# Kernel tuning notes

Measured on AMD Instinct MI355X. Metric: run time of the kernel, lower is better.

## Reference

```python
import jax, jax.numpy as jnp
import numpy as np

N_NODES = 50000
N_EDGES = 800000
NEG_SLOPE = 0.2


def _edge_softmax(scores, dst, n):
    # scores: [E, H]; softmax over edges grouped by destination node
    m = jax.ops.segment_max(scores, dst, num_segments=n)          # [N, H]
    ex = jnp.exp(scores - m[dst])                                 # [E, H]
    s = jax.ops.segment_sum(ex, dst, num_segments=n)              # [N, H]
    return ex / s[dst]


def _gat_layer(h, W, attn_l, attn_r, bias, src, dst, n, heads, out_d):
    feat = (h @ W).reshape(n, heads, out_d)                       # [N, H, D]
    el = jnp.sum(feat * attn_l, axis=-1)                          # [N, H]
    er = jnp.sum(feat * attn_r, axis=-1)                          # [N, H]
    e = jax.nn.leaky_relu(el[src] + er[dst], NEG_SLOPE)           # [E, H]
    alpha = _edge_softmax(e, dst, n)                              # [E, H]
    msg = feat[src] * alpha[:, :, None]                           # [E, H, D]
    rst = jax.ops.segment_sum(msg, dst, num_segments=n)           # [N, H, D]
    return rst + bias.reshape(1, heads, out_d)


def setup_inputs() -> dict:
    key = jax.random.key(0)
    ks = jax.random.split(key, 12)
    in_dim, hid, heads, out_dim = 128, 64, 4, 64
    sc = 0.1
    return {
        "emb": jax.random.normal(ks[0], (N_NODES, in_dim), jnp.float32),
        "src": jax.random.randint(ks[1], (N_EDGES,), 0, N_NODES, jnp.int32),
        "dst": jax.random.randint(ks[2], (N_EDGES,), 0, N_NODES, jnp.int32),
        "W1": jax.random.normal(ks[3], (in_dim, heads * hid), jnp.float32) * sc,
        "attn_l1": jax.random.normal(ks[4], (1, heads, hid), jnp.float32) * sc,
        "attn_r1": jax.random.normal(ks[5], (1, heads, hid), jnp.float32) * sc,
        "b1": jax.random.normal(ks[6], (heads * hid,), jnp.float32) * sc,
        "W2": jax.random.normal(ks[7], (heads * hid, out_dim), jnp.float32) * sc,
        "attn_l2": jax.random.normal(ks[8], (1, 1, out_dim), jnp.float32) * sc,
        "attn_r2": jax.random.normal(ks[9], (1, 1, out_dim), jnp.float32) * sc,
        "b2": jax.random.normal(ks[10], (out_dim,), jnp.float32) * sc,
    }


def reference(emb, src, dst, W1, attn_l1, attn_r1, b1, W2, attn_l2, attn_r2, b2):
    n = emb.shape[0]
    h = _gat_layer(emb, W1, attn_l1, attn_r1, b1, src, dst, n, 4, 64)   # [N,4,64]
    h = jax.nn.relu(h).reshape(n, 4 * 64)                                # [N,256]
    h = _gat_layer(h, W2, attn_l2, attn_r2, b2, src, dst, n, 1, 64)      # [N,1,64]
    return h.reshape(n, 64)
```

## Files before the change

kernel.cpp:

```cpp
#include <hip/hip_runtime.h>
#include <hip/hip_bf16.h>
#include <math.h>

#define DIV_UP(a,b) (((a)+(b)-1)/(b))

typedef __attribute__((ext_vector_type(8))) short short8v;
typedef __attribute__((ext_vector_type(4))) float f32x4;

__device__ __forceinline__ float bf_lo(unsigned u){ union{unsigned x; float f;} v; v.x = u << 16; return v.f; }
__device__ __forceinline__ float bf_hi(unsigned u){ union{unsigned x; float f;} v; v.x = u & 0xffff0000u; return v.f; }
__device__ __forceinline__ unsigned short f2bf(float f){
  union{float f; unsigned u;} v; v.f = f;
  unsigned r = v.u + 0x7fff + ((v.u >> 16) & 1);
  return (unsigned short)(r >> 16);
}
__device__ __forceinline__ unsigned packbf(float a, float b){
  return (unsigned)f2bf(a) | ((unsigned)f2bf(b) << 16);
}
__device__ __forceinline__ float lrelu(float x){ return x > 0.f ? x : 0.2f*x; }

__global__ __launch_bounds__(256) void k_scan1(const int* __restrict__ deg,
                                               int* __restrict__ blocksum, int N){
  int b = blockIdx.x;
  int base = b*1024 + threadIdx.x*4;
  int s = 0;
  if (base + 3 < N){
    int4 v = *(const int4*)&deg[base];
    s = v.x + v.y + v.z + v.w;
  } else {
    for (int i = 0; i < 4; i++){ int idx = base + i; if (idx < N) s += deg[idx]; }
  }
  #pragma unroll
  for (int o = 32; o; o >>= 1) s += __shfl_down(s, o);
  __shared__ int ws[4];
  int wid = threadIdx.x >> 6, lane = threadIdx.x & 63;
  if (lane == 0) ws[wid] = s;
  __syncthreads();
  if (threadIdx.x == 0) blocksum[b] = ws[0] + ws[1] + ws[2] + ws[3];
}

__global__ __launch_bounds__(256) void k_scan3(const int* __restrict__ deg,
                                               const int* __restrict__ blocksum, int nb,
                                               int* __restrict__ row_start,
                                               int* __restrict__ cursor, int N){
  int b = blockIdx.x;
  __shared__ int s_boff;
  if (threadIdx.x < 64){
    int acc = 0;
    for (int base = 0; base < nb; base += 64){
      int idx = base + threadIdx.x;
      if (idx < nb && idx < b) acc += blocksum[idx];
    }
    #pragma unroll
    for (int o = 32; o; o >>= 1) acc += __shfl_down(acc, o);
    if (threadIdx.x == 0) s_boff = acc;
  }
  int base = b*1024 + threadIdx.x*4;
  int v[4];
  #pragma unroll
  for (int i = 0; i < 4; i++){ int idx = base + i; v[i] = (idx < N) ? deg[idx] : 0; }
  int s = v[0] + v[1] + v[2] + v[3];
  int lane = threadIdx.x & 63, wid = threadIdx.x >> 6;
  int inc = s;
  #pragma unroll
  for (int o = 1; o < 64; o <<= 1){ int t = __shfl_up(inc, o); if (lane >= o) inc += t; }
  __shared__ int wsum[4];
  if (lane == 63) wsum[wid] = inc;
  __syncthreads();
  int woff = 0;
  #pragma unroll
  for (int i = 0; i < 4; i++) if (i < wid) woff += wsum[i];
  int run = s_boff + woff + inc - s;
  #pragma unroll
  for (int i = 0; i < 4; i++){
    int idx = base + i;
    if (idx < N){ row_start[idx] = run; cursor[idx] = run; run += v[i]; }
  }
  if (base < N && base + 4 >= N) row_start[N] = run;
}

__global__ void k_fillw4(const int* __restrict__ dst, const int* __restrict__ src,
                         int* __restrict__ cursor, int* __restrict__ srcp,
                         const float4* __restrict__ el4, const float4* __restrict__ er4,
                         float4* __restrict__ w4, int E){
  int i = blockIdx.x*blockDim.x + threadIdx.x;
  if (i < E){
    int d = dst[i], s = src[i];
    int p = atomicAdd(&cursor[d], 1);
    srcp[p] = s;
    float4 l = el4[s], r = er4[d];
    float4 w;
    w.x = __expf(lrelu(l.x + r.x));
    w.y = __expf(lrelu(l.y + r.y));
    w.z = __expf(lrelu(l.z + r.z));
    w.w = __expf(lrelu(l.w + r.w));
    w4[p] = w;
  }
}

__global__ __launch_bounds__(256) void k_gemm1_count(const float* __restrict__ A,
      const float* __restrict__ B,
      unsigned short* __restrict__ Cbf,
      const float* __restrict__ al, const float* __restrict__ ar,
      float* __restrict__ el, float* __restrict__ er, int M,
      const int* __restrict__ dst, int* __restrict__ deg, int E, int gemmBlocks){
  __shared__ alignas(16) __hip_bfloat16 At[64][136];
  __shared__ alignas(16) __hip_bfloat16 Bt[64][136];
  __shared__ float elp[2][64], erp[2][64];

  if (blockIdx.x >= gemmBlocks){
    int i = (blockIdx.x - gemmBlocks)*256 + threadIdx.x;
    if (i < E) atomicAdd(&deg[dst[i]], 1);
    return;
  }

  const int tid = threadIdx.x;
  const int lane = tid & 63, w = tid >> 6;
  const int mw = w >> 1, nw = w & 1;
  const int m0 = blockIdx.x * 64;
  const int rbase = mw*32, cbase = nw*32;
  const int fr = lane & 15, fg = lane >> 4;

  #pragma unroll
  for (int i = 0; i < 8; i++){
    int q = tid + i*256;
    int row = q >> 5, c4 = q & 31;
    float4 a = make_float4(0.f,0.f,0.f,0.f);
    if (m0 + row < M) a = *(const float4*)&A[(size_t)(m0+row)*128 + c4*4];
    *(uint2*)&At[row][c4*4] = make_uint2(packbf(a.x,a.y), packbf(a.z,a.w));
  }

  for (int by = 0; by < 4; by++){
    int n0 = by * 64;
    __syncthreads();
    #pragma unroll
    for (int i = 0; i < 8; i++){
      int q = tid + i*256;
      int c = q & 63, k4 = q >> 6;
      float b0 = B[(size_t)(k4*4+0)*256 + n0 + c];
      float b1 = B[(size_t)(k4*4+1)*256 + n0 + c];
      float b2 = B[(size_t)(k4*4+2)*256 + n0 + c];
      float b3 = B[(size_t)(k4*4+3)*256 + n0 + c];
      *(uint2*)&Bt[c][k4*4] = make_uint2(packbf(b0,b1), packbf(b2,b3));
    }
    __syncthreads();

    f32x4 acc[2][2];
    #pragma unroll
    for (int i = 0; i < 2; i++)
      #pragma unroll
      for (int jj = 0; jj < 2; jj++)
        #pragma unroll
        for (int r = 0; r < 4; r++) acc[i][jj][r] = 0.f;

    #pragma unroll
    for (int ks = 0; ks < 4; ks++){
      short8v a0 = *(const short8v*)&At[rbase + fr     ][ks*32 + fg*8];
      short8v a1 = *(const short8v*)&At[rbase + 16 + fr][ks*32 + fg*8];
      short8v b0 = *(const short8v*)&Bt[cbase + fr     ][ks*32 + fg*8];
      short8v b1 = *(const short8v*)&Bt[cbase + 16 + fr][ks*32 + fg*8];
      acc[0][0] = __builtin_amdgcn_mfma_f32_16x16x32_bf16(a0, b0, acc[0][0], 0,0,0);
      acc[0][1] = __builtin_amdgcn_mfma_f32_16x16x32_bf16(a0, b1, acc[0][1], 0,0,0);
      acc[1][0] = __builtin_amdgcn_mfma_f32_16x16x32_bf16(a1, b0, acc[1][0], 0,0,0);
      acc[1][1] = __builtin_amdgcn_mfma_f32_16x16x32_bf16(a1, b1, acc[1][1], 0,0,0);
    }

    float alv[2], arv[2];
    #pragma unroll
    for (int nt = 0; nt < 2; nt++){
      int col = cbase + nt*16 + fr;
      alv[nt] = al[n0 + col];
      arv[nt] = ar[n0 + col];
    }
    #pragma unroll
    for (int mt = 0; mt < 2; mt++){
      #pragma unroll
      for (int r = 0; r < 4; r++){
        float pl = acc[mt][0][r]*alv[0] + acc[mt][1][r]*alv[1];
        float pr = acc[mt][0][r]*arv[0] + acc[mt][1][r]*arv[1];
        #pragma unroll
        for (int o = 1; o < 16; o <<= 1){ pl += __shfl_xor(pl, o); pr += __shfl_xor(pr, o); }
        if (fr == 0){
          int rl = rbase + mt*16 + fg*4 + r;
          elp[nw][rl] = pl; erp[nw][rl] = pr;
        }
      }
    }
    #pragma unroll
    for (int mt = 0; mt < 2; mt++){
      #pragma unroll
      for (int r = 0; r < 4; r++){
        int row = m0 + rbase + mt*16 + fg*4 + r;
        if (row < M){
          #pragma unroll
          for (int nt = 0; nt < 2; nt++)
            Cbf[(size_t)row*256 + n0 + cbase + nt*16 + fr] = f2bf(acc[mt][nt][r]);
        }
      }
    }
    __syncthreads();
    if (tid < 64){
      int row = m0 + tid;
      if (row < M){
        el[(size_t)row*4 + by] = elp[0][tid] + elp[1][tid];
        er[(size_t)row*4 + by] = erp[0][tid] + erp[1][tid];
      }
    }
  }
}

template<int K, int H, bool ABF>
__global__ __launch_bounds__(256) void k_gemm_mfma(const void* __restrict__ Av,
      const float* __restrict__ B, int ldb,
      unsigned short* __restrict__ Cbf,
      const float* __restrict__ al, const float* __restrict__ ar,
      float* __restrict__ el, float* __restrict__ er, int M){
  constexpr int KP = K + 8;
  __shared__ alignas(16) __hip_bfloat16 At[64][KP];
  __shared__ alignas(16) __hip_bfloat16 Bt[64][KP];
  __shared__ float elp[2][64], erp[2][64];
  const int tid = threadIdx.x;
  const int lane = tid & 63, w = tid >> 6;
  const int mw = w >> 1, nw = w & 1;
  const int m0 = blockIdx.x * 64, by = blockIdx.y, n0 = by * 64;

  if constexpr (!ABF){
    const float* A = (const float*)Av;
    #pragma unroll
    for (int i = 0; i < K/16; i++){
      int q = tid + i*256;
      int row = q / (K/4), c4 = q % (K/4);
      float4 a = make_float4(0.f,0.f,0.f,0.f);
      if (m0 + row < M) a = *(const float4*)&A[(size_t)(m0+row)*K + c4*4];
      *(uint2*)&At[row][c4*4] = make_uint2(packbf(a.x,a.y), packbf(a.z,a.w));
    }
  } else {
    const __hip_bfloat16* A = (const __hip_bfloat16*)Av;
    #pragma unroll
    for (int i = 0; i < K/32; i++){
      int q = tid + i*256;
      int row = q / (K/8), c8 = q % (K/8);
      uint4 u = make_uint4(0,0,0,0);
      if (m0 + row < M) u = *(const uint4*)&A[(size_t)(m0+row)*K + c8*8];
      *(uint4*)&At[row][c8*8] = u;
    }
  }
  #pragma unroll
  for (int i = 0; i < K/16; i++){
    int q = tid + i*256;
    int c = q & 63, k4 = q >> 6;
    float b0 = B[(size_t)(k4*4+0)*ldb + n0 + c];
    float b1 = B[(size_t)(k4*4+1)*ldb + n0 + c];
    float b2 = B[(size_t)(k4*4+2)*ldb + n0 + c];
    float b3 = B[(size_t)(k4*4+3)*ldb + n0 + c];
    *(uint2*)&Bt[c][k4*4] = make_uint2(packbf(b0,b1), packbf(b2,b3));
  }
  __syncthreads();

  f32x4 acc[2][2];
  #pragma unroll
  for (int i = 0; i < 2; i++)
    #pragma unroll
    for (int j = 0; j < 2; j++)
      #pragma unroll
      for (int r = 0; r < 4; r++) acc[i][j][r] = 0.f;

  const int rbase = mw*32, cbase = nw*32;
  const int fr = lane & 15, fg = lane >> 4;
  #pragma unroll
  for (int ks = 0; ks < K/32; ks++){
    short8v a0 = *(const short8v*)&At[rbase + fr     ][ks*32 + fg*8];
    short8v a1 = *(const short8v*)&At[rbase + 16 + fr][ks*32 + fg*8];
    short8v b0 = *(const short8v*)&Bt[cbase + fr     ][ks*32 + fg*8];
    short8v b1 = *(const short8v*)&Bt[cbase + 16 + fr][ks*32 + fg*8];
    acc[0][0] = __builtin_amdgcn_mfma_f32_16x16x32_bf16(a0, b0, acc[0][0], 0,0,0);
    acc[0][1] = __builtin_amdgcn_mfma_f32_16x16x32_bf16(a0, b1, acc[0][1], 0,0,0);
    acc[1][0] = __builtin_amdgcn_mfma_f32_16x16x32_bf16(a1, b0, acc[1][0], 0,0,0);
    acc[1][1] = __builtin_amdgcn_mfma_f32_16x16x32_bf16(a1, b1, acc[1][1], 0,0,0);
  }

  float alv[2], arv[2];
  #pragma unroll
  for (int nt = 0; nt < 2; nt++){
    int col = cbase + nt*16 + fr;
    alv[nt] = al[by*64 + col];
    arv[nt] = ar[by*64 + col];
  }
  #pragma unroll
  for (int mt = 0; mt < 2; mt++){
    #pragma unroll
    for (int r = 0; r < 4; r++){
      float pl = acc[mt][0][r]*alv[0] + acc[mt][1][r]*alv[1];
      float pr = acc[mt][0][r]*arv[0] + acc[mt][1][r]*arv[1];
      #pragma unroll
      for (int o = 1; o < 16; o <<= 1){ pl += __shfl_xor(pl, o); pr += __shfl_xor(pr, o); }
      if (fr == 0){
        int rl = rbase + mt*16 + fg*4 + r;
        elp[nw][rl] = pl; erp[nw][rl] = pr;
      }
    }
  }
  const int NN = H*64;
  #pragma unroll
  for (int mt = 0; mt < 2; mt++){
    #pragma unroll
    for (int r = 0; r < 4; r++){
      int row = m0 + rbase + mt*16 + fg*4 + r;
      if (row < M){
        #pragma unroll
        for (int nt = 0; nt < 2; nt++)
          Cbf[(size_t)row*NN + n0 + cbase + nt*16 + fr] = f2bf(acc[mt][nt][r]);
      }
    }
  }
  __syncthreads();
  if (tid < 64){
    int row = m0 + tid;
    if (row < M){
      el[(size_t)row*H + by] = elp[0][tid] + elp[1][tid];
      er[(size_t)row*H + by] = erp[0][tid] + erp[1][tid];
    }
  }
}

__global__ __launch_bounds__(256) void k_gath4(const uint4* __restrict__ fbase,
      const float* __restrict__ w4, const int* __restrict__ row_start,
      const int* __restrict__ srcp, const float* __restrict__ bias,
      __hip_bfloat16* __restrict__ outb, int N, int nwaves){
  int wv = threadIdx.x >> 6, lane = threadIdx.x & 63;
  int g = lane >> 4, j = lane & 15, h = j >> 2;
  const unsigned jo2 = (unsigned)(j << 1);

  int n = blockIdx.x*4 + wv;
  if (n >= N) return;
  int rs = row_start[n], re = row_start[n+1];

  while (true){
    int deg = re - rs;
    int nn = n + nwaves;
    int rs_n = 0, re_n = 0;
    if (nn < N){ rs_n = row_start[nn]; re_n = row_start[nn+1]; }

    float acc[16];
    #pragma unroll
    for (int k = 0; k < 16; k++) acc[k] = 0.f;
    float Sacc = 0.f;

    int i = 0;
    int full = deg & ~15;
    for (; i < full; i += 16){
      float wb[4]; uint4 u0[4], u1[4];
      #pragma unroll
      for (int k = 0; k < 4; k++){
        unsigned e = (unsigned)(rs + i + k*4 + g);
        int sb = srcp[e];
        wb[k] = w4[(e << 2) + h];
        unsigned fi = ((unsigned)sb << 5) + jo2;
        u0[k] = fbase[fi];
        u1[k] = fbase[fi + 1];
      }
      #pragma unroll
      for (int k = 0; k < 4; k++){
        float wk = wb[k];
        Sacc += wk;
        acc[0]  += bf_lo(u0[k].x)*wk; acc[1]  += bf_hi(u0[k].x)*wk;
        acc[2]  += bf_lo(u0[k].y)*wk; acc[3]  += bf_hi(u0[k].y)*wk;
        acc[4]  += bf_lo(u0[k].z)*wk; acc[5]  += bf_hi(u0[k].z)*wk;
        acc[6]  += bf_lo(u0[k].w)*wk; acc[7]  += bf_hi(u0[k].w)*wk;
        acc[8]  += bf_lo(u1[k].x)*wk; acc[9]  += bf_hi(u1[k].x)*wk;
        acc[10] += bf_lo(u1[k].y)*wk; acc[11] += bf_hi(u1[k].y)*wk;
        acc[12] += bf_lo(u1[k].z)*wk; acc[13] += bf_hi(u1[k].z)*wk;
        acc[14] += bf_lo(u1[k].w)*wk; acc[15] += bf_hi(u1[k].w)*wk;
      }
    }
    if (i < deg){
      float wb[4]; uint4 u0[4], u1[4];
      #pragma unroll
      for (int k = 0; k < 4; k++){
        int e = i + k*4 + g;
        wb[k] = 0.f;
        u0[k] = make_uint4(0,0,0,0); u1[k] = make_uint4(0,0,0,0);
        if (e < deg){
          unsigned ee = (unsigned)(rs + e);
          int sb = srcp[ee];
          wb[k] = w4[(ee << 2) + h];
          unsigned fi = ((unsigned)sb << 5) + jo2;
          u0[k] = fbase[fi];
          u1[k] = fbase[fi + 1];
        }
      }
      #pragma unroll
      for (int k = 0; k < 4; k++){
        float wk = wb[k];
        Sacc += wk;
        acc[0]  += bf_lo(u0[k].x)*wk; acc[1]  += bf_hi(u0[k].x)*wk;
        acc[2]  += bf_lo(u0[k].y)*wk; acc[3]  += bf_hi(u0[k].y)*wk;
        acc[4]  += bf_lo(u0[k].z)*wk; acc[5]  += bf_hi(u0[k].z)*wk;
        acc[6]  += bf_lo(u0[k].w)*wk; acc[7]  += bf_hi(u0[k].w)*wk;
        acc[8]  += bf_lo(u1[k].x)*wk; acc[9]  += bf_hi(u1[k].x)*wk;
        acc[10] += bf_lo(u1[k].y)*wk; acc[11] += bf_hi(u1[k].y)*wk;
        acc[12] += bf_lo(u1[k].z)*wk; acc[13] += bf_hi(u1[k].z)*wk;
        acc[14] += bf_lo(u1[k].w)*wk; acc[15] += bf_hi(u1[k].w)*wk;
      }
    }

    #pragma unroll
    for (int k = 0; k < 16; k++){
      acc[k] += __shfl_xor(acc[k], 16);
      acc[k] += __shfl_xor(acc[k], 32);
    }
    Sacc += __shfl_xor(Sacc, 16);
    Sacc += __shfl_xor(Sacc, 32);
    if (g == 0){
      float inv = (deg > 0 && Sacc > 0.f) ? 1.f / Sacc : 0.f;
      float4 b0 = *(const float4*)&bias[j*16 + 0];
      float4 b1 = *(const float4*)&bias[j*16 + 4];
      float4 b2 = *(const float4*)&bias[j*16 + 8];
      float4 b3 = *(const float4*)&bias[j*16 + 12];
      float v[16];
      v[0]=acc[0]*inv+b0.x;  v[1]=acc[1]*inv+b0.y;  v[2]=acc[2]*inv+b0.z;  v[3]=acc[3]*inv+b0.w;
      v[4]=acc[4]*inv+b1.x;  v[5]=acc[5]*inv+b1.y;  v[6]=acc[6]*inv+b1.z;  v[7]=acc[7]*inv+b1.w;
      v[8]=acc[8]*inv+b2.x;  v[9]=acc[9]*inv+b2.y;  v[10]=acc[10]*inv+b2.z; v[11]=acc[11]*inv+b2.w;
      v[12]=acc[12]*inv+b3.x; v[13]=acc[13]*inv+b3.y; v[14]=acc[14]*inv+b3.z; v[15]=acc[15]*inv+b3.w;
      #pragma unroll
      for (int k = 0; k < 16; k++) v[k] = fmaxf(v[k], 0.f);
      uint4 o0, o1;
      o0.x = packbf(v[0], v[1]);   o0.y = packbf(v[2], v[3]);
      o0.z = packbf(v[4], v[5]);   o0.w = packbf(v[6], v[7]);
      o1.x = packbf(v[8], v[9]);   o1.y = packbf(v[10], v[11]);
      o1.z = packbf(v[12], v[13]); o1.w = packbf(v[14], v[15]);
      uint4* op = (uint4*)outb + (size_t)n*32 + (j << 1);
      op[0] = o0; op[1] = o1;
    }

    if (nn >= N) break;
    n = nn; rs = rs_n; re = re_n;
  }
}

__global__ __launch_bounds__(256) void k_gath1(const uint2* __restrict__ fbase,
      const float* __restrict__ el2, const float* __restrict__ er2,
      const int* __restrict__ row_start, const int* __restrict__ srcp,
      const float* __restrict__ bias, float* __restrict__ out, int N, int nwaves){
  int wv = threadIdx.x >> 6, lane = threadIdx.x & 63;
  int g = lane >> 4, j = lane & 15;
  const unsigned jo = (unsigned)j;

  int n = blockIdx.x*4 + wv;
  if (n >= N) return;
  int rs = row_start[n], re = row_start[n+1];

  while (true){
    int deg = re - rs;
    int nn = n + nwaves;
    int rs_n = 0, re_n = 0;
    if (nn < N){ rs_n = row_start[nn]; re_n = row_start[nn+1]; }

    float ern = er2[n];
    float acc[4] = {0.f, 0.f, 0.f, 0.f};
    float Sacc = 0.f;

    int i = 0;
    int full = deg & ~15;
    for (; i < full; i += 16){
      float wb[4]; uint2 u[4];
      #pragma unroll
      for (int k = 0; k < 4; k++){
        unsigned e = (unsigned)(rs + i + k*4 + g);
        int sb = srcp[e];
        float x = el2[sb] + ern;
        x = x > 0.f ? x : 0.2f*x;
        wb[k] = __expf(x);
        u[k] = fbase[((unsigned)sb << 4) + jo];
      }
      #pragma unroll
      for (int k = 0; k < 4; k++){
        float wk = wb[k];
        Sacc += wk;
        acc[0] += bf_lo(u[k].x)*wk; acc[1] += bf_hi(u[k].x)*wk;
        acc[2] += bf_lo(u[k].y)*wk; acc[3] += bf_hi(u[k].y)*wk;
      }
    }
    if (i < deg){
      float wb[4]; uint2 u[4];
      #pragma unroll
      for (int k = 0; k < 4; k++){
        int e = i + k*4 + g;
        wb[k] = 0.f;
        u[k] = make_uint2(0,0);
        if (e < deg){
          unsigned ee = (unsigned)(rs + e);
          int sb = srcp[ee];
          float x = el2[sb] + ern;
          x = x > 0.f ? x : 0.2f*x;
          wb[k] = __expf(x);
          u[k] = fbase[((unsigned)sb << 4) + jo];
        }
      }
      #pragma unroll
      for (int k = 0; k < 4; k++){
        float wk = wb[k];
        Sacc += wk;
        acc[0] += bf_lo(u[k].x)*wk; acc[1] += bf_hi(u[k].x)*wk;
        acc[2] += bf_lo(u[k].y)*wk; acc[3] += bf_hi(u[k].y)*wk;
      }
    }

    #pragma unroll
    for (int k = 0; k < 4; k++){
      acc[k] += __shfl_xor(acc[k], 16);
      acc[k] += __shfl_xor(acc[k], 32);
    }
    Sacc += __shfl_xor(Sacc, 16);
    Sacc += __shfl_xor(Sacc, 32);
    if (g == 0){
      float inv = (deg > 0 && Sacc > 0.f) ? 1.f / Sacc : 0.f;
      float4 b = *(const float4*)&bias[j*4];
      float4 o;
      o.x = acc[0]*inv + b.x; o.y = acc[1]*inv + b.y;
      o.z = acc[2]*inv + b.z; o.w = acc[3]*inv + b.w;
      *(float4*)&out[(size_t)n*64 + j*4] = o;
    }

    if (nn >= N) break;
    n = nn; rs = rs_n; re = re_n;
  }
}

extern "C" void kernel_launch(void* const* d_in, const int* in_sizes, int n_in,
                              void* d_out, int out_size, void* d_ws, size_t ws_size,
                              hipStream_t stream) {
  const float* emb = (const float*)d_in[0];
  const int*   src = (const int*)d_in[1];
  const int*   dst = (const int*)d_in[2];
  const float* W1  = (const float*)d_in[3];
  const float* al1 = (const float*)d_in[4];
  const float* ar1 = (const float*)d_in[5];
  const float* b1  = (const float*)d_in[6];
  const float* W2  = (const float*)d_in[7];
  const float* al2 = (const float*)d_in[8];
  const float* ar2 = (const float*)d_in[9];
  const float* b2  = (const float*)d_in[10];
  float* out = (float*)d_out;

  const int N = in_sizes[0] / 128;
  const int E = in_sizes[1];

  char* p = (char*)d_ws;
  auto alloc = [&](size_t bytes) -> void* {
    void* r = (void*)p; p += (bytes + 255) & ~(size_t)255; return r;
  };
  __hip_bfloat16* feat1b = (__hip_bfloat16*)alloc((size_t)N*256*2);
  __hip_bfloat16* h1b    = (__hip_bfloat16*)alloc((size_t)N*256*2);
  __hip_bfloat16* feat2b = (__hip_bfloat16*)alloc((size_t)N*64*2);
  float* el1             = (float*)alloc((size_t)N*4*4);
  float* er1             = (float*)alloc((size_t)N*4*4);
  float* el2             = (float*)alloc((size_t)N*4);
  float* er2             = (float*)alloc((size_t)N*4);
  int*   deg             = (int*)alloc((size_t)N*4);
  int*   row_start       = (int*)alloc((size_t)(N+1)*4);
  int*   cursor          = (int*)alloc((size_t)N*4);
  int*   blocksum        = (int*)alloc((size_t)DIV_UP(N,1024)*4);
  int*   srcp            = (int*)alloc((size_t)E*4);
  float* w4              = (float*)alloc((size_t)E*16);

  const int nb = DIV_UP(N, 1024);
  const int gblocks = min(DIV_UP(N, 4), 2048);
  const int nwaves  = gblocks * 4;
  const int gemmBlocks = DIV_UP(N, 64);
  const int cntBlocks  = DIV_UP(E, 256);

  hipMemsetAsync(deg, 0, (size_t)N*4, stream);

  k_gemm1_count<<<gemmBlocks + cntBlocks, 256, 0, stream>>>(
      emb, W1, (unsigned short*)feat1b, al1, ar1, el1, er1, N,
      dst, deg, E, gemmBlocks);

  k_scan1<<<nb, 256, 0, stream>>>(deg, blocksum, N);
  k_scan3<<<nb, 256, 0, stream>>>(deg, blocksum, nb, row_start, cursor, N);
  k_fillw4<<<DIV_UP(E,256), 256, 0, stream>>>(dst, src, cursor, srcp,
      (const float4*)el1, (const float4*)er1, (float4*)w4, E);

  k_gath4<<<gblocks, 256, 0, stream>>>((const uint4*)feat1b, w4, row_start,
                                       srcp, b1, h1b, N, nwaves);
  k_gemm_mfma<256,1,true><<<dim3(DIV_UP(N,64), 1), 256, 0, stream>>>(
      h1b, W2, 64, (unsigned short*)feat2b, al2, ar2, el2, er2, N);
  k_gath1<<<gblocks, 256, 0, stream>>>((const uint2*)feat2b, el2, er2,
                                       row_start, srcp, b2, out, N, nwaves);
}
```

Baseline: 200.0 us.

## Split gather kernels by feature column chunks and store edge weights per head

Edge attention weights are now stored head-major (one plane per head) instead of interleaved float4. Both aggregation kernels split the feature dimension into column chunks handled by separate blocks, so each wave covers 16 or 32 edges per iteration with a single 16-byte load per lane rather than several loads per lane. The aim is to cut register pressure and improve load coalescing. In exchange, srcp and the edge indices are re-read once per chunk, there are more shuffle reduction steps, and the grid sizes change.

```diff
diff --git a/kernel.cpp b/kernel.cpp
--- a/kernel.cpp
+++ b/kernel.cpp
@@ -82,19 +82,17 @@
 __global__ void k_fillw4(const int* __restrict__ dst, const int* __restrict__ src,
                          int* __restrict__ cursor, int* __restrict__ srcp,
                          const float4* __restrict__ el4, const float4* __restrict__ er4,
-                         float4* __restrict__ w4, int E){
+                         float* __restrict__ w4T, int E){
   int i = blockIdx.x*blockDim.x + threadIdx.x;
   if (i < E){
     int d = dst[i], s = src[i];
     int p = atomicAdd(&cursor[d], 1);
     srcp[p] = s;
     float4 l = el4[s], r = er4[d];
-    float4 w;
-    w.x = __expf(lrelu(l.x + r.x));
-    w.y = __expf(lrelu(l.y + r.y));
-    w.z = __expf(lrelu(l.z + r.z));
-    w.w = __expf(lrelu(l.w + r.w));
-    w4[p] = w;
+    w4T[0*E + p] = __expf(lrelu(l.x + r.x));
+    w4T[1*E + p] = __expf(lrelu(l.y + r.y));
+    w4T[2*E + p] = __expf(lrelu(l.z + r.z));
+    w4T[3*E + p] = __expf(lrelu(l.w + r.w));
   }
 }
 
@@ -323,15 +321,18 @@
   }
 }
 
-__global__ __launch_bounds__(256) void k_gath4(const uint4* __restrict__ fbase,
-      const float* __restrict__ w4, const int* __restrict__ row_start,
+__global__ __launch_bounds__(256) void k_gath4s(const uint4* __restrict__ fbase,
+      const float* __restrict__ w4T, const int* __restrict__ row_start,
       const int* __restrict__ srcp, const float* __restrict__ bias,
-      __hip_bfloat16* __restrict__ outb, int N, int nwaves){
+      __hip_bfloat16* __restrict__ outb, int N, int E, int nwaves){
   int wv = threadIdx.x >> 6, lane = threadIdx.x & 63;
-  int g = lane >> 4, j = lane & 15, h = j >> 2;
-  const unsigned jo2 = (unsigned)(j << 1);
-
-  int n = blockIdx.x*4 + wv;
+  int c = blockIdx.x & 7;
+  int h = c >> 1;
+  int el_ = lane >> 2, s = lane & 3;
+  const float* wplane = w4T + (size_t)h*E;
+  const unsigned cbase = (unsigned)(c << 2);
+
+  int n = (blockIdx.x >> 3)*4 + wv;
   if (n >= N) return;
   int rs = row_start[n], re = row_start[n+1];
 
@@ -341,96 +342,64 @@
     int rs_n = 0, re_n = 0;
     if (nn < N){ rs_n = row_start[nn]; re_n = row_start[nn+1]; }
 
-    float acc[16];
-    #pragma unroll
-    for (int k = 0; k < 16; k++) acc[k] = 0.f;
+    float acc[8];
+    #pragma unroll
+    for (int k = 0; k < 8; k++) acc[k] = 0.f;
     float Sacc = 0.f;
 
     int i = 0;
     int full = deg & ~15;
     for (; i < full; i += 16){
-      float wb[4]; uint4 u0[4], u1[4];
-      #pragma unroll
-      for (int k = 0; k < 4; k++){
-        unsigned e = (unsigned)(rs + i + k*4 + g);
-        int sb = srcp[e];
-        wb[k] = w4[(e << 2) + h];
-        unsigned fi = ((unsigned)sb << 5) + jo2;
-        u0[k] = fbase[fi];
-        u1[k] = fbase[fi + 1];
-      }
-      #pragma unroll
-      for (int k = 0; k < 4; k++){
-        float wk = wb[k];
-        Sacc += wk;
-        acc[0]  += bf_lo(u0[k].x)*wk; acc[1]  += bf_hi(u0[k].x)*wk;
-        acc[2]  += bf_lo(u0[k].y)*wk; acc[3]  += bf_hi(u0[k].y)*wk;
-        acc[4]  += bf_lo(u0[k].z)*wk; acc[5]  += bf_hi(u0[k].z)*wk;
-        acc[6]  += bf_lo(u0[k].w)*wk; acc[7]  += bf_hi(u0[k].w)*wk;
-        acc[8]  += bf_lo(u1[k].x)*wk; acc[9]  += bf_hi(u1[k].x)*wk;
-        acc[10] += bf_lo(u1[k].y)*wk; acc[11] += bf_hi(u1[k].y)*wk;
-        acc[12] += bf_lo(u1[k].z)*wk; acc[13] += bf_hi(u1[k].z)*wk;
-        acc[14] += bf_lo(u1[k].w)*wk; acc[15] += bf_hi(u1[k].w)*wk;
-      }
+      unsigned ee = (unsigned)(rs + i + el_);
+      int sb = srcp[ee];
+      float w = wplane[ee];
+      uint4 u = fbase[((unsigned)sb << 5) + cbase + s];
+      Sacc += w;
+      acc[0] += bf_lo(u.x)*w; acc[1] += bf_hi(u.x)*w;
+      acc[2] += bf_lo(u.y)*w; acc[3] += bf_hi(u.y)*w;
+      acc[4] += bf_lo(u.z)*w; acc[5] += bf_hi(u.z)*w;
+      acc[6] += bf_lo(u.w)*w; acc[7] += bf_hi(u.w)*w;
     }
     if (i < deg){
-      float wb[4]; uint4 u0[4], u1[4];
-      #pragma unroll
-      for (int k = 0; k < 4; k++){
-        int e = i + k*4 + g;
-        wb[k] = 0.f;
-        u0[k] = make_uint4(0,0,0,0); u1[k] = make_uint4(0,0,0,0);
-        if (e < deg){
-          unsigned ee = (unsigned)(rs + e);
-          int sb = srcp[ee];
-          wb[k] = w4[(ee << 2) + h];
-          unsigned fi = ((unsigned)sb << 5) + jo2;
-          u0[k] = fbase[fi];
-          u1[k] = fbase[fi + 1];
-        }
-      }
-      #pragma unroll
-      for (int k = 0; k < 4; k++){
-        float wk = wb[k];
-        Sacc += wk;
-        acc[0]  += bf_lo(u0[k].x)*wk; acc[1]  += bf_hi(u0[k].x)*wk;
-        acc[2]  += bf_lo(u0[k].y)*wk; acc[3]  += bf_hi(u0[k].y)*wk;
-        acc[4]  += bf_lo(u0[k].z)*wk; acc[5]  += bf_hi(u0[k].z)*wk;
-        acc[6]  += bf_lo(u0[k].w)*wk; acc[7]  += bf_hi(u0[k].w)*wk;
-        acc[8]  += bf_lo(u1[k].x)*wk; acc[9]  += bf_hi(u1[k].x)*wk;
-        acc[10] += bf_lo(u1[k].y)*wk; acc[11] += bf_hi(u1[k].y)*wk;
-        acc[12] += bf_lo(u1[k].z)*wk; acc[13] += bf_hi(u1[k].z)*wk;
-        acc[14] += bf_lo(u1[k].w)*wk; acc[15] += bf_hi(u1[k].w)*wk;
-      }
-    }
-
-    #pragma unroll
-    for (int k = 0; k < 16; k++){
-      acc[k] += __shfl_xor(acc[k], 16);
-      acc[k] += __shfl_xor(acc[k], 32);
-    }
-    Sacc += __shfl_xor(Sacc, 16);
-    Sacc += __shfl_xor(Sacc, 32);
-    if (g == 0){
+      int e = i + el_;
+      float w = 0.f; uint4 u = make_uint4(0,0,0,0);
+      if (e < deg){
+        unsigned ee = (unsigned)(rs + e);
+        int sb = srcp[ee];
+        w = wplane[ee];
+        u = fbase[((unsigned)sb << 5) + cbase + s];
+      }
+      Sacc += w;
+      acc[0] += bf_lo(u.x)*w; acc[1] += bf_hi(u.x)*w;
+      acc[2] += bf_lo(u.y)*w; acc[3] += bf_hi(u.y)*w;
+      acc[4] += bf_lo(u.z)*w; acc[5] += bf_hi(u.z)*w;
+      acc[6] += bf_lo(u.w)*w; acc[7] += bf_hi(u.w)*w;
+    }
+
+    #pragma unroll
+    for (int o = 4; o < 64; o <<= 1){
+      #pragma unroll
+      for (int k = 0; k < 8; k++) acc[k] += __shfl_xor(acc[k], o);
+      Sacc += __shfl_xor(Sacc, o);
+    }
+
+    if (el_ == 0){
       float inv = (deg > 0 && Sacc > 0.f) ? 1.f / Sacc : 0.f;
-      float4 b0 = *(const float4*)&bias[j*16 + 0];
-      float4 b1 = *(const float4*)&bias[j*16 + 4];
-      float4 b2 = *(const float4*)&bias[j*16 + 8];
-      float4 b3 = *(const float4*)&bias[j*16 + 12];
-      float v[16];
-      v[0]=acc[0]*inv+b0.x;  v[1]=acc[1]*inv+b0.y;  v[2]=acc[2]*inv+b0.z;  v[3]=acc[3]*inv+b0.w;
-      v[4]=acc[4]*inv+b1.x;  v[5]=acc[5]*inv+b1.y;  v[6]=acc[6]*inv+b1.z;  v[7]=acc[7]*inv+b1.w;
-      v[8]=acc[8]*inv+b2.x;  v[9]=acc[9]*inv+b2.y;  v[10]=acc[10]*inv+b2.z; v[11]=acc[11]*inv+b2.w;
-      v[12]=acc[12]*inv+b3.x; v[13]=acc[13]*inv+b3.y; v[14]=acc[14]*inv+b3.z; v[15]=acc[15]*inv+b3.w;
-      #pragma unroll
-      for (int k = 0; k < 16; k++) v[k] = fmaxf(v[k], 0.f);
-      uint4 o0, o1;
-      o0.x = packbf(v[0], v[1]);   o0.y = packbf(v[2], v[3]);
-      o0.z = packbf(v[4], v[5]);   o0.w = packbf(v[6], v[7]);
-      o1.x = packbf(v[8], v[9]);   o1.y = packbf(v[10], v[11]);
-      o1.z = packbf(v[12], v[13]); o1.w = packbf(v[14], v[15]);
-      uint4* op = (uint4*)outb + (size_t)n*32 + (j << 1);
-      op[0] = o0; op[1] = o1;
+      int d0 = c*32 + s*8;
+      float4 b0 = *(const float4*)&bias[d0];
+      float4 b1 = *(const float4*)&bias[d0 + 4];
+      float v0 = fmaxf(acc[0]*inv + b0.x, 0.f);
+      float v1 = fmaxf(acc[1]*inv + b0.y, 0.f);
+      float v2 = fmaxf(acc[2]*inv + b0.z, 0.f);
+      float v3 = fmaxf(acc[3]*inv + b0.w, 0.f);
+      float v4 = fmaxf(acc[4]*inv + b1.x, 0.f);
+      float v5 = fmaxf(acc[5]*inv + b1.y, 0.f);
+      float v6 = fmaxf(acc[6]*inv + b1.z, 0.f);
+      float v7 = fmaxf(acc[7]*inv + b1.w, 0.f);
+      uint4 o;
+      o.x = packbf(v0, v1); o.y = packbf(v2, v3);
+      o.z = packbf(v4, v5); o.w = packbf(v6, v7);
+      ((uint4*)outb)[(size_t)n*32 + cbase + s] = o;
     }
 
     if (nn >= N) break;
@@ -438,15 +407,16 @@
   }
 }
 
-__global__ __launch_bounds__(256) void k_gath1(const uint2* __restrict__ fbase,
+__global__ __launch_bounds__(256) void k_gath1s(const uint4* __restrict__ fbase,
       const float* __restrict__ el2, const float* __restrict__ er2,
       const int* __restrict__ row_start, const int* __restrict__ srcp,
       const float* __restrict__ bias, float* __restrict__ out, int N, int nwaves){
   int wv = threadIdx.x >> 6, lane = threadIdx.x & 63;
-  int g = lane >> 4, j = lane & 15;
-  const unsigned jo = (unsigned)j;
-
-  int n = blockIdx.x*4 + wv;
+  int c = blockIdx.x & 3;
+  int el_ = lane >> 1, s = lane & 1;
+  const unsigned cbase = (unsigned)(c << 1);
+
+  int n = (blockIdx.x >> 2)*4 + wv;
   if (n >= N) return;
   int rs = row_start[n], re = row_start[n+1];
 
@@ -457,69 +427,63 @@
     if (nn < N){ rs_n = row_start[nn]; re_n = row_start[nn+1]; }
 
     float ern = er2[n];
-    float acc[4] = {0.f, 0.f, 0.f, 0.f};
+    float acc[8];
+    #pragma unroll
+    for (int k = 0; k < 8; k++) acc[k] = 0.f;
     float Sacc = 0.f;
 
     int i = 0;
-    int full = deg & ~15;
-    for (; i < full; i += 16){
-      float wb[4]; uint2 u[4];
-      #pragma unroll
-      for (int k = 0; k < 4; k++){
-        unsigned e = (unsigned)(rs + i + k*4 + g);
-        int sb = srcp[e];
+    int full = deg & ~31;
+    for (; i < full; i += 32){
+      unsigned ee = (unsigned)(rs + i + el_);
+      int sb = srcp[ee];
+      float x = el2[sb] + ern;
+      x = x > 0.f ? x : 0.2f*x;
+      float w = __expf(x);
+      uint4 u = fbase[((unsigned)sb << 3) + cbase + s];
+      Sacc += w;
+      acc[0] += bf_lo(u.x)*w; acc[1] += bf_hi(u.x)*w;
+      acc[2] += bf_lo(u.y)*w; acc[3] += bf_hi(u.y)*w;
+      acc[4] += bf_lo(u.z)*w; acc[5] += bf_hi(u.z)*w;
+      acc[6] += bf_lo(u.w)*w; acc[7] += bf_hi(u.w)*w;
+    }
+    if (i < deg){
+      int e = i + el_;
+      float w = 0.f; uint4 u = make_uint4(0,0,0,0);
+      if (e < deg){
+        unsigned ee = (unsigned)(rs + e);
+        int sb = srcp[ee];
         float x = el2[sb] + ern;
         x = x > 0.f ? x : 0.2f*x;
-        wb[k] = __expf(x);
-        u[k] = fbase[((unsigned)sb << 4) + jo];
-      }
-      #pragma unroll
-      for (int k = 0; k < 4; k++){
-        float wk = wb[k];
-        Sacc += wk;
-        acc[0] += bf_lo(u[k].x)*wk; acc[1] += bf_hi(u[k].x)*wk;
-        acc[2] += bf_lo(u[k].y)*wk; acc[3] += bf_hi(u[k].y)*wk;
-      }
-    }
-    if (i < deg){
-      float wb[4]; uint2 u[4];
-      #pragma unroll
-      for (int k = 0; k < 4; k++){
-        int e = i + k*4 + g;
-        wb[k] = 0.f;
-        u[k] = make_uint2(0,0);
-        if (e < deg){
-          unsigned ee = (unsigned)(rs + e);
-          int sb = srcp[ee];
-          float x = el2[sb] + ern;
-          x = x > 0.f ? x : 0.2f*x;
-          wb[k] = __expf(x);
-          u[k] = fbase[((unsigned)sb << 4) + jo];
-        }
-      }
-      #pragma unroll
-      for (int k = 0; k < 4; k++){
-        float wk = wb[k];
-        Sacc += wk;
-        acc[0] += bf_lo(u[k].x)*wk; acc[1] += bf_hi(u[k].x)*wk;
-        acc[2] += bf_lo(u[k].y)*wk; acc[3] += bf_hi(u[k].y)*wk;
-      }
-    }
-
-    #pragma unroll
-    for (int k = 0; k < 4; k++){
-      acc[k] += __shfl_xor(acc[k], 16);
-      acc[k] += __shfl_xor(acc[k], 32);
-    }
-    Sacc += __shfl_xor(Sacc, 16);
-    Sacc += __shfl_xor(Sacc, 32);
-    if (g == 0){
+        w = __expf(x);
+        u = fbase[((unsigned)sb << 3) + cbase + s];
+      }
+      Sacc += w;
+      acc[0] += bf_lo(u.x)*w; acc[1] += bf_hi(u.x)*w;
+      acc[2] += bf_lo(u.y)*w; acc[3] += bf_hi(u.y)*w;
+      acc[4] += bf_lo(u.z)*w; acc[5] += bf_hi(u.z)*w;
+      acc[6] += bf_lo(u.w)*w; acc[7] += bf_hi(u.w)*w;
+    }
+
+    #pragma unroll
+    for (int o = 2; o < 64; o <<= 1){
+      #pragma unroll
+      for (int k = 0; k < 8; k++) acc[k] += __shfl_xor(acc[k], o);
+      Sacc += __shfl_xor(Sacc, o);
+    }
+
+    if (el_ == 0){
       float inv = (deg > 0 && Sacc > 0.f) ? 1.f / Sacc : 0.f;
-      float4 b = *(const float4*)&bias[j*4];
-      float4 o;
-      o.x = acc[0]*inv + b.x; o.y = acc[1]*inv + b.y;
-      o.z = acc[2]*inv + b.z; o.w = acc[3]*inv + b.w;
-      *(float4*)&out[(size_t)n*64 + j*4] = o;
+      int d0 = c*16 + s*8;
+      float4 b0 = *(const float4*)&bias[d0];
+      float4 b1 = *(const float4*)&bias[d0 + 4];
+      float4 o0, o1;
+      o0.x = acc[0]*inv + b0.x; o0.y = acc[1]*inv + b0.y;
+      o0.z = acc[2]*inv + b0.z; o0.w = acc[3]*inv + b0.w;
+      o1.x = acc[4]*inv + b1.x; o1.y = acc[5]*inv + b1.y;
+      o1.z = acc[6]*inv + b1.z; o1.w = acc[7]*inv + b1.w;
+      *(float4*)&out[(size_t)n*64 + d0] = o0;
+      *(float4*)&out[(size_t)n*64 + d0 + 4] = o1;
     }
 
     if (nn >= N) break;
@@ -562,13 +526,16 @@
   int*   cursor          = (int*)alloc((size_t)N*4);
   int*   blocksum        = (int*)alloc((size_t)DIV_UP(N,1024)*4);
   int*   srcp            = (int*)alloc((size_t)E*4);
-  float* w4              = (float*)alloc((size_t)E*16);
+  float* w4T             = (float*)alloc((size_t)E*4*4);
 
   const int nb = DIV_UP(N, 1024);
-  const int gblocks = min(DIV_UP(N, 4), 2048);
-  const int nwaves  = gblocks * 4;
   const int gemmBlocks = DIV_UP(N, 64);
   const int cntBlocks  = DIV_UP(E, 256);
+
+  const int g4nodeblk = 256;
+  const int g4nwaves  = g4nodeblk * 4;
+  const int g1nodeblk = 512;
+  const int g1nwaves  = g1nodeblk * 4;
 
   hipMemsetAsync(deg, 0, (size_t)N*4, stream);
 
@@ -579,12 +546,12 @@
   k_scan1<<<nb, 256, 0, stream>>>(deg, blocksum, N);
   k_scan3<<<nb, 256, 0, stream>>>(deg, blocksum, nb, row_start, cursor, N);
   k_fillw4<<<DIV_UP(E,256), 256, 0, stream>>>(dst, src, cursor, srcp,
-      (const float4*)el1, (const float4*)er1, (float4*)w4, E);
-
-  k_gath4<<<gblocks, 256, 0, stream>>>((const uint4*)feat1b, w4, row_start,
-                                       srcp, b1, h1b, N, nwaves);
+      (const float4*)el1, (const float4*)er1, w4T, E);
+
+  k_gath4s<<<8 * g4nodeblk, 256, 0, stream>>>((const uint4*)feat1b, w4T, row_start,
+                                              srcp, b1, h1b, N, E, g4nwaves);
   k_gemm_mfma<256,1,true><<<dim3(DIV_UP(N,64), 1), 256, 0, stream>>>(
       h1b, W2, 64, (unsigned short*)feat2b, al2, ar2, el2, er2, N);
-  k_gath1<<<gblocks, 256, 0, stream>>>((const uint2*)feat2b, el2, er2,
-                                       row_start, srcp, b2, out, N, nwaves);
-}
+  k_gath1s<<<4 * g1nodeblk, 256, 0, stream>>>((const uint4*)feat2b, el2, er2,
+                                              row_start, srcp, b2, out, N, g1nwaves);
+}
```

After: 425.3 us. 2.13x slower.
